# Optimization experiments

Measured on AMD Instinct MI355X. Metric: run time of the kernel, lower is better.

## Reference

```python
import jax, jax.numpy as jnp
import numpy as np

NB, DIM, DSTATE, DCONV, EXPAND = 4, 256, 16, 4, 2
DIN = EXPAND * DIM                 # 512
DTRANK = (DIM + 15) // 16          # 16, mamba-ssm default dt_rank = ceil(d_model/16)
B, L = 16, 512


def layer_norm(x, w, b, eps=1e-5):
    mu = x.mean(-1, keepdims=True)
    var = x.var(-1, keepdims=True)
    return (x - mu) * jax.lax.rsqrt(var + eps) * w + b


def selective_scan(u, delta, A, Bm, Cm, D):
    # u, delta: (B,L,DIN); Bm,Cm: (B,L,N); A: (DIN,N); D: (DIN,)
    def step(h, xs):
        d_t, B_t, C_t, u_t = xs          # (B,DIN), (B,N), (B,N), (B,DIN)
        dA = jnp.exp(d_t[..., None] * A)                                  # (B,DIN,N)
        h = dA * h + d_t[..., None] * B_t[:, None, :] * u_t[..., None]   # (B,DIN,N)
        y = jnp.einsum('bdn,bn->bd', h, C_t)
        return h, y

    h0 = jnp.zeros((u.shape[0], u.shape[2], A.shape[1]), u.dtype)
    xs = (delta.transpose(1, 0, 2), Bm.transpose(1, 0, 2),
          Cm.transpose(1, 0, 2), u.transpose(1, 0, 2))
    _, ys = jax.lax.scan(step, h0, xs)
    return ys.transpose(1, 0, 2) + u * D


def mamba_block(x, ln_w, ln_b, in_w, in_b, cw, cb, xp_w, dtw, dtb, A_log, D, ow):
    h = layer_norm(x, ln_w, ln_b)
    xz = h @ in_w.T + in_b                       # (B,L,2*DIN)
    xin, z = xz[..., :DIN], xz[..., DIN:]
    # causal depthwise conv over the sequence dim
    xc = jax.lax.conv_general_dilated(
        xin.transpose(0, 2, 1), cw[:, None, :], (1,), [(DCONV - 1, 0)],
        dimension_numbers=('NCH', 'OIH', 'NCH'), feature_group_count=DIN)
    xc = jax.nn.silu(xc + cb[None, :, None]).transpose(0, 2, 1)   # (B,L,DIN)
    dbc = xc @ xp_w.T                                             # (B,L,DTRANK+2*N)
    dt = jax.nn.softplus(dbc[..., :DTRANK] @ dtw.T + dtb)         # (B,L,DIN)
    Bm = dbc[..., DTRANK:DTRANK + DSTATE]
    Cm = dbc[..., DTRANK + DSTATE:]
    y = selective_scan(xc, dt, -jnp.exp(A_log), Bm, Cm, D)
    return x + (y * jax.nn.silu(z)) @ ow.T       # dropout = identity at eval


def setup_inputs() -> dict:
    key = jax.random.key(0)
    ks = jax.random.split(key, 8)
    s = 0.02
    A_log = jnp.tile(jnp.log(jnp.arange(1, DSTATE + 1, dtype=jnp.float32))[None, None, :],
                     (NB, DIN, 1))
    return {
        'x': jax.random.normal(ks[0], (B, L, DIM), jnp.float32),
        'ln_w': jnp.ones((NB, DIM), jnp.float32),
        'ln_b': jnp.zeros((NB, DIM), jnp.float32),
        'in_proj_w': jax.random.normal(ks[1], (NB, 2 * DIN, DIM), jnp.float32) * s,
        'in_proj_b': jnp.zeros((NB, 2 * DIN), jnp.float32),
        'conv_w': jax.random.normal(ks[2], (NB, DIN, DCONV), jnp.float32) * s,
        'conv_b': jnp.zeros((NB, DIN), jnp.float32),
        'x_proj_w': jax.random.normal(ks[3], (NB, DTRANK + 2 * DSTATE, DIN), jnp.float32) * s,
        'dt_proj_w': jax.random.normal(ks[4], (NB, DIN, DTRANK), jnp.float32) * s,
        'dt_proj_b': jax.random.uniform(ks[5], (NB, DIN), jnp.float32, -4.0, -3.0),
        'A_log': A_log,
        'D': jnp.ones((NB, DIN), jnp.float32),
        'out_proj_w': jax.random.normal(ks[6], (NB, DIM, DIN), jnp.float32) * s,
    }


def reference(x, ln_w, ln_b, in_proj_w, in_proj_b, conv_w, conv_b, x_proj_w,
              dt_proj_w, dt_proj_b, A_log, D, out_proj_w):
    for i in range(NB):
        x = mamba_block(x, ln_w[i], ln_b[i], in_proj_w[i], in_proj_b[i],
                        conv_w[i], conv_b[i], x_proj_w[i], dt_proj_w[i],
                        dt_proj_b[i], A_log[i], D[i], out_proj_w[i])
    return x
```

## Files before the change

### kernel.cpp

```cpp
#include <hip/hip_runtime.h>
#include <math.h>

#define NB 4
#define DIMM 256
#define DSTATE 16
#define DCONV 4
#define DIN 512
#define DTRANK 16
#define BB 16
#define LL 512
#define TT (BB * LL)
#define XZ_DIM (2 * DIN)
#define DBC_DIM (DTRANK + 2 * DSTATE)
#define NC 32
#define CHUNK (LL / NC)

__device__ __forceinline__ unsigned short f2bf(float f) {
    union { float f; unsigned int u; } v; v.f = f;
    unsigned int r = v.u + 0x7fff + ((v.u >> 16) & 1);
    return (unsigned short)(r >> 16);
}
__device__ __forceinline__ float bf2f(unsigned short u) {
    union { unsigned int i; float f; } v; v.i = ((unsigned int)u) << 16;
    return v.f;
}

__global__ __launch_bounds__(256) void cvt3_kernel(const float* __restrict__ s1,
                                                   unsigned short* __restrict__ d1, int n1,
                                                   const float* __restrict__ s2,
                                                   unsigned short* __restrict__ d2, int n2,
                                                   const float* __restrict__ s3,
                                                   unsigned short* __restrict__ d3, int n3) {
    int stride = gridDim.x * 256;
    for (int i = blockIdx.x * 256 + threadIdx.x; i < n1; i += stride) {
        float4 v = ((const float4*)s1)[i];
        ushort4 o; o.x = f2bf(v.x); o.y = f2bf(v.y); o.z = f2bf(v.z); o.w = f2bf(v.w);
        ((ushort4*)d1)[i] = o;
    }
    for (int i = blockIdx.x * 256 + threadIdx.x; i < n2; i += stride) {
        float4 v = ((const float4*)s2)[i];
        ushort4 o; o.x = f2bf(v.x); o.y = f2bf(v.y); o.z = f2bf(v.z); o.w = f2bf(v.w);
        ((ushort4*)d2)[i] = o;
    }
    for (int i = blockIdx.x * 256 + threadIdx.x; i < n3; i += stride) {
        float4 v = ((const float4*)s3)[i];
        ushort4 o; o.x = f2bf(v.x); o.y = f2bf(v.y); o.z = f2bf(v.z); o.w = f2bf(v.w);
        ((ushort4*)d3)[i] = o;
    }
}

__global__ __launch_bounds__(256) void ln_kernel(const float* __restrict__ x,
                                                 const float* __restrict__ w,
                                                 const float* __restrict__ bvec,
                                                 unsigned short* __restrict__ out) {
    int t = blockIdx.x;
    int i = threadIdx.x;
    float v = x[t * DIMM + i];
    float s = v, s2 = v * v;
#pragma unroll
    for (int off = 1; off < 64; off <<= 1) {
        s  += __shfl_xor(s, off);
        s2 += __shfl_xor(s2, off);
    }
    __shared__ float ss[4], ss2[4];
    int wid = i >> 6;
    if ((i & 63) == 0) { ss[wid] = s; ss2[wid] = s2; }
    __syncthreads();
    s  = ss[0] + ss[1] + ss[2] + ss[3];
    s2 = ss2[0] + ss2[1] + ss2[2] + ss2[3];
    float mu  = s * (1.0f / DIMM);
    float var = s2 * (1.0f / DIMM) - mu * mu;
    float r   = rsqrtf(var + 1e-5f);
    out[t * DIMM + i] = f2bf((v - mu) * r * w[i] + bvec[i]);
}

#define GBM2 128
#define GBN2 128
#define GBK2 32
#define LDW2 (GBK2 + 8)
__global__ __launch_bounds__(256) void gemm128(const unsigned short* __restrict__ A, int lda,
                                               const unsigned short* __restrict__ Bw, int ldb,
                                               const float* __restrict__ bias,
                                               unsigned short* __restrict__ C1b,
                                               unsigned short* __restrict__ C2b, int nsplit,
                                               int ldc, int K) {
    using short8  = __attribute__((ext_vector_type(8))) short;
    using floatx4 = __attribute__((ext_vector_type(4))) float;
    __shared__ __align__(16) unsigned short As[GBM2 * LDW2];
    __shared__ __align__(16) unsigned short Bs[GBN2 * LDW2];

    int tid  = threadIdx.x;
    int m0   = blockIdx.y * GBM2;
    int n0   = blockIdx.x * GBN2;
    int w    = tid >> 6;
    int lane = tid & 63;
    int wm   = (w & 1) * 64;
    int wn   = (w >> 1) * 64;
    int lr   = lane & 15;
    int quad = lane >> 4;

    floatx4 acc[4][4] = {};

    int ar = tid >> 1;
    int ak = (tid & 1) * 16;

    for (int k0 = 0; k0 < K; k0 += GBK2) {
        {
            const unsigned short* src = &A[(size_t)(m0 + ar) * lda + k0 + ak];
            int4 a0 = *(const int4*)(src);
            int4 a1 = *(const int4*)(src + 8);
            *(int4*)&As[ar * LDW2 + ak]     = a0;
            *(int4*)&As[ar * LDW2 + ak + 8] = a1;
        }
        {
            const unsigned short* src = &Bw[(size_t)(n0 + ar) * ldb + k0 + ak];
            int4 b0 = *(const int4*)(src);
            int4 b1 = *(const int4*)(src + 8);
            *(int4*)&Bs[ar * LDW2 + ak]     = b0;
            *(int4*)&Bs[ar * LDW2 + ak + 8] = b1;
        }
        __syncthreads();
        short8 af[4], bf[4];
#pragma unroll
        for (int i = 0; i < 4; ++i)
            af[i] = *(const short8*)&As[(wm + i * 16 + lr) * LDW2 + quad * 8];
#pragma unroll
        for (int j = 0; j < 4; ++j)
            bf[j] = *(const short8*)&Bs[(wn + j * 16 + lr) * LDW2 + quad * 8];
#pragma unroll
        for (int i = 0; i < 4; ++i)
#pragma unroll
            for (int j = 0; j < 4; ++j)
                acc[i][j] = __builtin_amdgcn_mfma_f32_16x16x32_bf16(af[i], bf[j], acc[i][j], 0, 0, 0);
        __syncthreads();
    }

#pragma unroll
    for (int j = 0; j < 4; ++j) {
        int cn = n0 + wn + j * 16 + lr;
        float bb = bias ? bias[cn] : 0.0f;
        unsigned short* dst = (cn < nsplit) ? C1b : C2b;
        int col = (cn < nsplit) ? cn : cn - nsplit;
#pragma unroll
        for (int i = 0; i < 4; ++i)
#pragma unroll
            for (int r = 0; r < 4; ++r) {
                int cm = m0 + wm + i * 16 + quad * 4 + r;
                dst[(size_t)cm * ldc + col] = f2bf(acc[i][j][r] + bb);
            }
    }
}

#define TBM 128
#define TBN 64
#define TBK 32
#define LDKW (TBK + 8)
__global__ __launch_bounds__(256) void gemm_bf16(const unsigned short* __restrict__ A, int lda,
                                                 const unsigned short* __restrict__ Bw, int ldb,
                                                 const float* __restrict__ bias,
                                                 const float* __restrict__ resid,
                                                 float* __restrict__ C,
                                                 unsigned short* __restrict__ C1b,
                                                 unsigned short* __restrict__ C2b, int nsplit,
                                                 int ldc, int N, int K) {
    using short8  = __attribute__((ext_vector_type(8))) short;
    using floatx4 = __attribute__((ext_vector_type(4))) float;
    __shared__ __align__(16) unsigned short As[TBM * LDKW];
    __shared__ __align__(16) unsigned short Bs[TBN * LDKW];

    int tid  = threadIdx.x;
    int m0   = blockIdx.y * TBM;
    int n0   = blockIdx.x * TBN;
    int w    = tid >> 6;
    int lane = tid & 63;
    int wm   = (w & 1) * 64;
    int wn   = (w >> 1) * 32;
    int lr   = lane & 15;
    int quad = lane >> 4;

    floatx4 acc[4][2] = {};

    int ar = tid >> 1;
    int ak = (tid & 1) * 16;
    int br = tid >> 2;
    int bk = (tid & 3) * 8;

    for (int k0 = 0; k0 < K; k0 += TBK) {
        {
            const unsigned short* src = &A[(size_t)(m0 + ar) * lda + k0 + ak];
            int4 a0 = *(const int4*)(src);
            int4 a1 = *(const int4*)(src + 8);
            *(int4*)&As[ar * LDKW + ak]     = a0;
            *(int4*)&As[ar * LDKW + ak + 8] = a1;
        }
        {
            int gn = n0 + br;
            int4 b0 = make_int4(0, 0, 0, 0);
            if (gn < N) b0 = *(const int4*)&Bw[(size_t)gn * ldb + k0 + bk];
            *(int4*)&Bs[br * LDKW + bk] = b0;
        }
        __syncthreads();
        short8 af[4], bf[2];
#pragma unroll
        for (int i = 0; i < 4; ++i)
            af[i] = *(const short8*)&As[(wm + i * 16 + lr) * LDKW + quad * 8];
#pragma unroll
        for (int j = 0; j < 2; ++j)
            bf[j] = *(const short8*)&Bs[(wn + j * 16 + lr) * LDKW + quad * 8];
#pragma unroll
        for (int i = 0; i < 4; ++i)
#pragma unroll
            for (int j = 0; j < 2; ++j)
                acc[i][j] = __builtin_amdgcn_mfma_f32_16x16x32_bf16(af[i], bf[j], acc[i][j], 0, 0, 0);
        __syncthreads();
    }

#pragma unroll
    for (int j = 0; j < 2; ++j) {
        int cn = n0 + wn + j * 16 + lr;
        if (cn < N) {
            float bb = bias ? bias[cn] : 0.0f;
            if (C1b) {
                unsigned short* dst = (cn < nsplit) ? C1b : C2b;
                int col = (cn < nsplit) ? cn : cn - nsplit;
#pragma unroll
                for (int i = 0; i < 4; ++i)
#pragma unroll
                    for (int r = 0; r < 4; ++r) {
                        int cm = m0 + wm + i * 16 + quad * 4 + r;
                        dst[(size_t)cm * ldc + col] = f2bf(acc[i][j][r] + bb);
                    }
            } else {
#pragma unroll
                for (int i = 0; i < 4; ++i)
#pragma unroll
                    for (int r = 0; r < 4; ++r) {
                        int cm = m0 + wm + i * 16 + quad * 4 + r;
                        float v = acc[i][j][r] + bb;
                        if (resid) v += resid[(size_t)cm * ldc + cn];
                        C[(size_t)cm * ldc + cn] = v;
                    }
            }
        }
    }
}

__global__ __launch_bounds__(256) void conv_silu(const unsigned short* __restrict__ Xb,
                                                 const float* __restrict__ cw,
                                                 const float* __restrict__ cb,
                                                 unsigned short* __restrict__ xcb) {
    int idx = blockIdx.x * blockDim.x + threadIdx.x;
    int d = idx & (DIN - 1);
    int t = idx >> 9;
    int l = t & (LL - 1);
    int bq = t >> 9;
    float acc = cb[d];
#pragma unroll
    for (int k = 0; k < DCONV; ++k) {
        int ls = l - (DCONV - 1) + k;
        if (ls >= 0) acc += cw[d * DCONV + k] * bf2f(Xb[(size_t)(bq * LL + ls) * DIN + d]);
    }
    float v = acc / (1.0f + __expf(-acc));
    xcb[(size_t)t * DIN + d] = f2bf(v);
}

__global__ __launch_bounds__(256) void dt_kernel(const float* __restrict__ dbc,
                                                 const float* __restrict__ dtw,
                                                 const float* __restrict__ dtbias,
                                                 unsigned short* __restrict__ dtout) {
    int idx = blockIdx.x * blockDim.x + threadIdx.x;
    int d = idx & (DIN - 1);
    int t = idx >> 9;
    float a = dtbias[d];
    const float4* wv = (const float4*)(dtw + d * DTRANK);
    const float* dr = dbc + (size_t)t * DBC_DIM;
#pragma unroll
    for (int q = 0; q < 4; ++q) {
        float4 w4 = wv[q];
        a += w4.x * dr[q * 4 + 0] + w4.y * dr[q * 4 + 1] +
             w4.z * dr[q * 4 + 2] + w4.w * dr[q * 4 + 3];
    }
    float sp = (a > 20.0f) ? a : log1pf(__expf(a));
    dtout[(size_t)t * DIN + d] = f2bf(sp);
}

__global__ __launch_bounds__(256) void scan_p1(const unsigned short* __restrict__ xcb,
                                               const unsigned short* __restrict__ dtb,
                                               const float* __restrict__ dbc,
                                               const float* __restrict__ A_log,
                                               float* __restrict__ S,
                                               float* __restrict__ H) {
    int bid = blockIdx.x;
    int dq = bid & 3;
    int c  = (bid >> 2) & (NC - 1);
    int b  = bid >> 7;
    int dloc = threadIdx.x >> 1;
    int sh   = threadIdx.x & 1;
    int d  = dq * 128 + dloc;
    int n0 = sh * 8;
    int base = b * LL + c * CHUNK;

    __shared__ float LB[CHUNK * DBC_DIM];
    for (int i = threadIdx.x; i < CHUNK * DBC_DIM / 4; i += 256)
        ((float4*)LB)[i] = ((const float4*)(dbc + (size_t)base * DBC_DIM))[i];

    float a[8];
    {
        const float4* ar = (const float4*)(A_log + d * DSTATE + n0);
        float4 v0 = ar[0], v1 = ar[1];
        a[0] = -__expf(v0.x); a[1] = -__expf(v0.y); a[2] = -__expf(v0.z); a[3] = -__expf(v0.w);
        a[4] = -__expf(v1.x); a[5] = -__expf(v1.y); a[6] = -__expf(v1.z); a[7] = -__expf(v1.w);
    }
    __syncthreads();

    float h[8];
#pragma unroll
    for (int j = 0; j < 8; ++j) h[j] = 0.0f;
    float Ssum = 0.0f;
    float u   = bf2f(xcb[(size_t)base * DIN + d]);
    float dtv = bf2f(dtb[(size_t)base * DIN + d]);
#pragma unroll 4
    for (int s = 0; s < CHUNK; ++s) {
        float nu  = bf2f(xcb[(size_t)(base + s + 1) * DIN + d]);
        float ndt = bf2f(dtb[(size_t)(base + s + 1) * DIN + d]);
        const float* row = &LB[s * DBC_DIM];
        float4 b0 = *(const float4*)&row[DTRANK + n0];
        float4 b1 = *(const float4*)&row[DTRANK + n0 + 4];
        const float btv[8] = {b0.x, b0.y, b0.z, b0.w, b1.x, b1.y, b1.z, b1.w};
        Ssum += dtv;
        float wv = dtv * u;
#pragma unroll
        for (int j = 0; j < 8; ++j) {
            float dA = __expf(dtv * a[j]);
            h[j] = dA * h[j] + wv * btv[j];
        }
        u = nu; dtv = ndt;
    }
    size_t sc = (size_t)b * NC + c;
    if (sh == 0) S[sc * DIN + d] = Ssum;
#pragma unroll
    for (int j = 0; j < 8; ++j) H[(sc * DIN + d) * 16 + n0 + j] = h[j];
}

__global__ __launch_bounds__(256) void scan_p2(const float* __restrict__ A_log,
                                               const float* __restrict__ S,
                                               float* __restrict__ H) {
    int idx = blockIdx.x * 256 + threadIdx.x;
    int n = idx & 15;
    int d = (idx >> 4) & (DIN - 1);
    int b = idx >> 13;
    float a = -__expf(A_log[d * DSTATE + n]);
    float h = 0.0f;
#pragma unroll
    for (int c = 0; c < NC; ++c) {
        size_t sc = (size_t)b * NC + c;
        float Sv = S[sc * DIN + d];
        size_t q = (sc * DIN + d) * 16 + n;
        float Hc = H[q];
        H[q] = h;
        h = __expf(a * Sv) * h + Hc;
    }
}

__global__ __launch_bounds__(256) void scan_p3(const unsigned short* __restrict__ xcb,
                                               const unsigned short* __restrict__ dtb,
                                               const unsigned short* __restrict__ Zb,
                                               const float* __restrict__ dbc,
                                               const float* __restrict__ A_log,
                                               const float* __restrict__ Dp,
                                               const float* __restrict__ Hin,
                                               unsigned short* __restrict__ gb) {
    int bid = blockIdx.x;
    int dq = bid & 3;
    int c  = (bid >> 2) & (NC - 1);
    int b  = bid >> 7;
    int dloc = threadIdx.x >> 1;
    int sh   = threadIdx.x & 1;
    int d  = dq * 128 + dloc;
    int n0 = sh * 8;
    int base = b * LL + c * CHUNK;

    __shared__ float LB[CHUNK * DBC_DIM];
    for (int i = threadIdx.x; i < CHUNK * DBC_DIM / 4; i += 256)
        ((float4*)LB)[i] = ((const float4*)(dbc + (size_t)base * DBC_DIM))[i];

    float a[8];
    {
        const float4* ar = (const float4*)(A_log + d * DSTATE + n0);
        float4 v0 = ar[0], v1 = ar[1];
        a[0] = -__expf(v0.x); a[1] = -__expf(v0.y); a[2] = -__expf(v0.z); a[3] = -__expf(v0.w);
        a[4] = -__expf(v1.x); a[5] = -__expf(v1.y); a[6] = -__expf(v1.z); a[7] = -__expf(v1.w);
    }
    float Dd = Dp[d];
    size_t sc = (size_t)b * NC + c;
    float h[8];
#pragma unroll
    for (int j = 0; j < 8; ++j) h[j] = Hin[(sc * DIN + d) * 16 + n0 + j];
    __syncthreads();

    float u   = bf2f(xcb[(size_t)base * DIN + d]);
    float dtv = bf2f(dtb[(size_t)base * DIN + d]);
#pragma unroll 4
    for (int s = 0; s < CHUNK; ++s) {
        float nu  = bf2f(xcb[(size_t)(base + s + 1) * DIN + d]);
        float ndt = bf2f(dtb[(size_t)(base + s + 1) * DIN + d]);
        const float* row = &LB[s * DBC_DIM];
        float4 b0 = *(const float4*)&row[DTRANK + n0];
        float4 b1 = *(const float4*)&row[DTRANK + n0 + 4];
        float4 c0 = *(const float4*)&row[DTRANK + DSTATE + n0];
        float4 c1 = *(const float4*)&row[DTRANK + DSTATE + n0 + 4];
        const float btv[8] = {b0.x, b0.y, b0.z, b0.w, b1.x, b1.y, b1.z, b1.w};
        const float ctv[8] = {c0.x, c0.y, c0.z, c0.w, c1.x, c1.y, c1.z, c1.w};
        float wv = dtv * u;
        float y  = (sh == 0) ? u * Dd : 0.0f;
#pragma unroll
        for (int j = 0; j < 8; ++j) {
            float dA = __expf(dtv * a[j]);
            h[j] = dA * h[j] + wv * btv[j];
            y += h[j] * ctv[j];
        }
        y += __shfl_xor(y, 1);
        if (sh == 0) {
            float zf = bf2f(Zb[(size_t)(base + s) * DIN + d]);
            float g = y * (zf / (1.0f + __expf(-zf)));
            gb[(size_t)(base + s) * DIN + d] = f2bf(g);
        }
        u = nu; dtv = ndt;
    }
}

extern "C" void kernel_launch(void* const* d_in, const int* in_sizes, int n_in,
                              void* d_out, int out_size, void* d_ws, size_t ws_size,
                              hipStream_t stream) {
    const float* x_in   = (const float*)d_in[0];
    const float* ln_w   = (const float*)d_in[1];
    const float* ln_b   = (const float*)d_in[2];
    const float* in_w   = (const float*)d_in[3];
    const float* in_b   = (const float*)d_in[4];
    const float* conv_w = (const float*)d_in[5];
    const float* conv_b = (const float*)d_in[6];
    const float* xp_w   = (const float*)d_in[7];
    const float* dt_w   = (const float*)d_in[8];
    const float* dt_b   = (const float*)d_in[9];
    const float* A_log  = (const float*)d_in[10];
    const float* Dp     = (const float*)d_in[11];
    const float* ow     = (const float*)d_in[12];
    float* out = (float*)d_out;

    const size_t M = 1048576;
    float* ws = (float*)d_ws;
    float* xbuf = ws;
    unsigned short* hb  = (unsigned short*)(ws + 2 * M);
    float* dbc = ws + 3 * M;
    unsigned short* Xb  = (unsigned short*)(ws + 4 * M);
    unsigned short* Zb  = (unsigned short*)(ws + 6 * M);
    unsigned short* xcb = (unsigned short*)(ws + 8 * M);
    unsigned short* dtb = (unsigned short*)(ws + 10 * M);
    unsigned short* gb  = (unsigned short*)(ws + 12 * M);
    float* Hbuf = ws + 14 * M;
    float* Sbuf = ws + 18 * M;
    unsigned short* inwb = (unsigned short*)(ws + 18 * M + 262144);
    unsigned short* owb  = inwb + (size_t)NB * XZ_DIM * DIMM;
    unsigned short* xpwb = owb + (size_t)NB * DIMM * DIN;

    cvt3_kernel<<<256, 256, 0, stream>>>(
        in_w, inwb, NB * XZ_DIM * DIMM / 4,
        ow,   owb,  NB * DIMM * DIN / 4,
        xp_w, xpwb, NB * DBC_DIM * DIN / 4);

    for (int layer = 0; layer < NB; ++layer) {
        const float* xi = (layer == 0) ? x_in : xbuf;
        float* xo = (layer == NB - 1) ? out : xbuf;

        ln_kernel<<<TT, 256, 0, stream>>>(xi, ln_w + layer * DIMM, ln_b + layer * DIMM, hb);

        gemm128<<<dim3(XZ_DIM / GBN2, TT / GBM2), 256, 0, stream>>>(
            hb, DIMM, inwb + (size_t)layer * XZ_DIM * DIMM, DIMM,
            in_b + layer * XZ_DIM, Xb, Zb, DIN, DIN, DIMM);

        conv_silu<<<(TT * DIN) / 256, 256, 0, stream>>>(
            Xb, conv_w + layer * DIN * DCONV, conv_b + layer * DIN, xcb);

        gemm_bf16<<<dim3(1, TT / TBM), 256, 0, stream>>>(
            xcb, DIN, xpwb + (size_t)layer * DBC_DIM * DIN, DIN,
            nullptr, nullptr, dbc, nullptr, nullptr, 0, DBC_DIM, DBC_DIM, DIN);

        dt_kernel<<<(TT * DIN) / 256, 256, 0, stream>>>(
            dbc, dt_w + (size_t)layer * DIN * DTRANK, dt_b + layer * DIN, dtb);

        const float* Al = A_log + (size_t)layer * DIN * DSTATE;
        scan_p1<<<BB * NC * 4, 256, 0, stream>>>(xcb, dtb, dbc, Al, Sbuf, Hbuf);
        scan_p2<<<(BB * DIN * 16) / 256, 256, 0, stream>>>(Al, Sbuf, Hbuf);
        scan_p3<<<BB * NC * 4, 256, 0, stream>>>(xcb, dtb, Zb, dbc, Al,
                                                 Dp + layer * DIN, Hbuf, gb);

        gemm_bf16<<<dim3(DIMM / TBN, TT / TBM), 256, 0, stream>>>(
            gb, DIN, owb + (size_t)layer * DIMM * DIN, DIN,
            nullptr, xi, xo, nullptr, nullptr, 0, DIMM, DIMM, DIN);
    }
}
```

Before: 679.3 us.

## Fuse dt projection into scan kernels, specialize x/out-proj GEMMs, vectorize layernorm

Measured after the change: 623.0 us. 8.3% less time.

```diff
diff --git a/kernel.cpp b/kernel.cpp
--- a/kernel.cpp
+++ b/kernel.cpp
@@ -49,29 +49,32 @@
     }
 }
 
-__global__ __launch_bounds__(256) void ln_kernel(const float* __restrict__ x,
-                                                 const float* __restrict__ w,
-                                                 const float* __restrict__ bvec,
-                                                 unsigned short* __restrict__ out) {
-    int t = blockIdx.x;
-    int i = threadIdx.x;
-    float v = x[t * DIMM + i];
-    float s = v, s2 = v * v;
+__global__ __launch_bounds__(256) void ln_kernel2(const float* __restrict__ x,
+                                                  const float* __restrict__ w,
+                                                  const float* __restrict__ bvec,
+                                                  unsigned short* __restrict__ out) {
+    int wid  = threadIdx.x >> 6;
+    int lane = threadIdx.x & 63;
+    int t = blockIdx.x * 4 + wid;
+    float4 v = *(const float4*)&x[(size_t)t * DIMM + lane * 4];
+    float s  = v.x + v.y + v.z + v.w;
+    float s2 = v.x * v.x + v.y * v.y + v.z * v.z + v.w * v.w;
 #pragma unroll
     for (int off = 1; off < 64; off <<= 1) {
         s  += __shfl_xor(s, off);
         s2 += __shfl_xor(s2, off);
     }
-    __shared__ float ss[4], ss2[4];
-    int wid = i >> 6;
-    if ((i & 63) == 0) { ss[wid] = s; ss2[wid] = s2; }
-    __syncthreads();
-    s  = ss[0] + ss[1] + ss[2] + ss[3];
-    s2 = ss2[0] + ss2[1] + ss2[2] + ss2[3];
     float mu  = s * (1.0f / DIMM);
     float var = s2 * (1.0f / DIMM) - mu * mu;
     float r   = rsqrtf(var + 1e-5f);
-    out[t * DIMM + i] = f2bf((v - mu) * r * w[i] + bvec[i]);
+    float4 w4 = *(const float4*)&w[lane * 4];
+    float4 b4 = *(const float4*)&bvec[lane * 4];
+    ushort4 o;
+    o.x = f2bf((v.x - mu) * r * w4.x + b4.x);
+    o.y = f2bf((v.y - mu) * r * w4.y + b4.y);
+    o.z = f2bf((v.z - mu) * r * w4.z + b4.z);
+    o.w = f2bf((v.w - mu) * r * w4.w + b4.w);
+    *(ushort4*)&out[(size_t)t * DIMM + lane * 4] = o;
 }
 
 #define GBM2 128
@@ -151,100 +154,6 @@
     }
 }
 
-#define TBM 128
-#define TBN 64
-#define TBK 32
-#define LDKW (TBK + 8)
-__global__ __launch_bounds__(256) void gemm_bf16(const unsigned short* __restrict__ A, int lda,
-                                                 const unsigned short* __restrict__ Bw, int ldb,
-                                                 const float* __restrict__ bias,
-                                                 const float* __restrict__ resid,
-                                                 float* __restrict__ C,
-                                                 unsigned short* __restrict__ C1b,
-                                                 unsigned short* __restrict__ C2b, int nsplit,
-                                                 int ldc, int N, int K) {
-    using short8  = __attribute__((ext_vector_type(8))) short;
-    using floatx4 = __attribute__((ext_vector_type(4))) float;
-    __shared__ __align__(16) unsigned short As[TBM * LDKW];
-    __shared__ __align__(16) unsigned short Bs[TBN * LDKW];
-
-    int tid  = threadIdx.x;
-    int m0   = blockIdx.y * TBM;
-    int n0   = blockIdx.x * TBN;
-    int w    = tid >> 6;
-    int lane = tid & 63;
-    int wm   = (w & 1) * 64;
-    int wn   = (w >> 1) * 32;
-    int lr   = lane & 15;
-    int quad = lane >> 4;
-
-    floatx4 acc[4][2] = {};
-
-    int ar = tid >> 1;
-    int ak = (tid & 1) * 16;
-    int br = tid >> 2;
-    int bk = (tid & 3) * 8;
-
-    for (int k0 = 0; k0 < K; k0 += TBK) {
-        {
-            const unsigned short* src = &A[(size_t)(m0 + ar) * lda + k0 + ak];
-            int4 a0 = *(const int4*)(src);
-            int4 a1 = *(const int4*)(src + 8);
-            *(int4*)&As[ar * LDKW + ak]     = a0;
-            *(int4*)&As[ar * LDKW + ak + 8] = a1;
-        }
-        {
-            int gn = n0 + br;
-            int4 b0 = make_int4(0, 0, 0, 0);
-            if (gn < N) b0 = *(const int4*)&Bw[(size_t)gn * ldb + k0 + bk];
-            *(int4*)&Bs[br * LDKW + bk] = b0;
-        }
-        __syncthreads();
-        short8 af[4], bf[2];
-#pragma unroll
-        for (int i = 0; i < 4; ++i)
-            af[i] = *(const short8*)&As[(wm + i * 16 + lr) * LDKW + quad * 8];
-#pragma unroll
-        for (int j = 0; j < 2; ++j)
-            bf[j] = *(const short8*)&Bs[(wn + j * 16 + lr) * LDKW + quad * 8];
-#pragma unroll
-        for (int i = 0; i < 4; ++i)
-#pragma unroll
-            for (int j = 0; j < 2; ++j)
-                acc[i][j] = __builtin_amdgcn_mfma_f32_16x16x32_bf16(af[i], bf[j], acc[i][j], 0, 0, 0);
-        __syncthreads();
-    }
-
-#pragma unroll
-    for (int j = 0; j < 2; ++j) {
-        int cn = n0 + wn + j * 16 + lr;
-        if (cn < N) {
-            float bb = bias ? bias[cn] : 0.0f;
-            if (C1b) {
-                unsigned short* dst = (cn < nsplit) ? C1b : C2b;
-                int col = (cn < nsplit) ? cn : cn - nsplit;
-#pragma unroll
-                for (int i = 0; i < 4; ++i)
-#pragma unroll
-                    for (int r = 0; r < 4; ++r) {
-                        int cm = m0 + wm + i * 16 + quad * 4 + r;
-                        dst[(size_t)cm * ldc + col] = f2bf(acc[i][j][r] + bb);
-                    }
-            } else {
-#pragma unroll
-                for (int i = 0; i < 4; ++i)
-#pragma unroll
-                    for (int r = 0; r < 4; ++r) {
-                        int cm = m0 + wm + i * 16 + quad * 4 + r;
-                        float v = acc[i][j][r] + bb;
-                        if (resid) v += resid[(size_t)cm * ldc + cn];
-                        C[(size_t)cm * ldc + cn] = v;
-                    }
-            }
-        }
-    }
-}
-
 __global__ __launch_bounds__(256) void conv_silu(const unsigned short* __restrict__ Xb,
                                                  const float* __restrict__ cw,
                                                  const float* __restrict__ cb,
@@ -264,30 +173,115 @@
     xcb[(size_t)t * DIN + d] = f2bf(v);
 }
 
-__global__ __launch_bounds__(256) void dt_kernel(const float* __restrict__ dbc,
-                                                 const float* __restrict__ dtw,
-                                                 const float* __restrict__ dtbias,
-                                                 unsigned short* __restrict__ dtout) {
-    int idx = blockIdx.x * blockDim.x + threadIdx.x;
-    int d = idx & (DIN - 1);
-    int t = idx >> 9;
-    float a = dtbias[d];
-    const float4* wv = (const float4*)(dtw + d * DTRANK);
-    const float* dr = dbc + (size_t)t * DBC_DIM;
-#pragma unroll
-    for (int q = 0; q < 4; ++q) {
-        float4 w4 = wv[q];
-        a += w4.x * dr[q * 4 + 0] + w4.y * dr[q * 4 + 1] +
-             w4.z * dr[q * 4 + 2] + w4.w * dr[q * 4 + 3];
-    }
-    float sp = (a > 20.0f) ? a : log1pf(__expf(a));
-    dtout[(size_t)t * DIN + d] = f2bf(sp);
+#define XPM 64
+__global__ __launch_bounds__(256) void xproj_gemm(const unsigned short* __restrict__ A,
+                                                  const unsigned short* __restrict__ Bw,
+                                                  float* __restrict__ dbc) {
+    using short8  = __attribute__((ext_vector_type(8))) short;
+    using floatx4 = __attribute__((ext_vector_type(4))) float;
+    __shared__ __align__(16) unsigned short As[XPM * DIN];
+    __shared__ __align__(16) unsigned short Bs[48 * DIN];
+
+    int tid = threadIdx.x;
+    int m0  = blockIdx.x * XPM;
+#pragma unroll
+    for (int t = 0; t < 16; ++t) {
+        int i = tid + t * 256;
+        int r = i >> 6, c = i & 63;
+        int col = (c * 8) ^ ((r & 7) << 3);
+        *(int4*)&As[r * DIN + col] = *(const int4*)&A[(size_t)(m0 + r) * DIN + c * 8];
+    }
+#pragma unroll
+    for (int t = 0; t < 12; ++t) {
+        int i = tid + t * 256;
+        int r = i >> 6, c = i & 63;
+        int col = (c * 8) ^ ((r & 7) << 3);
+        *(int4*)&Bs[r * DIN + col] = *(const int4*)&Bw[(size_t)r * DIN + c * 8];
+    }
+    __syncthreads();
+
+    int w = tid >> 6, lane = tid & 63, lr = lane & 15, quad = lane >> 4;
+    int wm = w * 16;
+    floatx4 acc[3] = {};
+#pragma unroll
+    for (int k0 = 0; k0 < DIN; k0 += 32) {
+        int ca = (k0 + quad * 8) ^ ((lr & 7) << 3);
+        short8 af = *(const short8*)&As[(wm + lr) * DIN + ca];
+        short8 b0 = *(const short8*)&Bs[(0  + lr) * DIN + ca];
+        short8 b1 = *(const short8*)&Bs[(16 + lr) * DIN + ca];
+        short8 b2 = *(const short8*)&Bs[(32 + lr) * DIN + ca];
+        acc[0] = __builtin_amdgcn_mfma_f32_16x16x32_bf16(af, b0, acc[0], 0, 0, 0);
+        acc[1] = __builtin_amdgcn_mfma_f32_16x16x32_bf16(af, b1, acc[1], 0, 0, 0);
+        acc[2] = __builtin_amdgcn_mfma_f32_16x16x32_bf16(af, b2, acc[2], 0, 0, 0);
+    }
+#pragma unroll
+    for (int j = 0; j < 3; ++j) {
+        int cn = j * 16 + lr;
+#pragma unroll
+        for (int r = 0; r < 4; ++r) {
+            int row = wm + quad * 4 + r;
+            dbc[(size_t)(m0 + row) * DBC_DIM + cn] = acc[j][r];
+        }
+    }
+}
+
+__global__ __launch_bounds__(256) void oproj_gemm(const unsigned short* __restrict__ A,
+                                                  const unsigned short* __restrict__ Bw,
+                                                  const float* __restrict__ resid,
+                                                  float* __restrict__ C) {
+    using short8  = __attribute__((ext_vector_type(8))) short;
+    using floatx4 = __attribute__((ext_vector_type(4))) float;
+    __shared__ __align__(16) unsigned short As[64 * DIN];
+    __shared__ __align__(16) unsigned short Bs[64 * DIN];
+
+    int tid = threadIdx.x;
+    int m0  = blockIdx.y * 64;
+    int n0  = blockIdx.x * 64;
+#pragma unroll
+    for (int t = 0; t < 16; ++t) {
+        int i = tid + t * 256;
+        int r = i >> 6, c = i & 63;
+        int col = (c * 8) ^ ((r & 7) << 3);
+        *(int4*)&As[r * DIN + col] = *(const int4*)&A[(size_t)(m0 + r) * DIN + c * 8];
+    }
+#pragma unroll
+    for (int t = 0; t < 16; ++t) {
+        int i = tid + t * 256;
+        int r = i >> 6, c = i & 63;
+        int col = (c * 8) ^ ((r & 7) << 3);
+        *(int4*)&Bs[r * DIN + col] = *(const int4*)&Bw[(size_t)(n0 + r) * DIN + c * 8];
+    }
+    __syncthreads();
+
+    int w = tid >> 6, lane = tid & 63, lr = lane & 15, quad = lane >> 4;
+    int wm = w * 16;
+    floatx4 acc[4] = {};
+#pragma unroll
+    for (int k0 = 0; k0 < DIN; k0 += 32) {
+        int ca = (k0 + quad * 8) ^ ((lr & 7) << 3);
+        short8 af = *(const short8*)&As[(wm + lr) * DIN + ca];
+#pragma unroll
+        for (int j = 0; j < 4; ++j) {
+            short8 bf = *(const short8*)&Bs[(j * 16 + lr) * DIN + ca];
+            acc[j] = __builtin_amdgcn_mfma_f32_16x16x32_bf16(af, bf, acc[j], 0, 0, 0);
+        }
+    }
+#pragma unroll
+    for (int j = 0; j < 4; ++j) {
+        int cn = n0 + j * 16 + lr;
+#pragma unroll
+        for (int r = 0; r < 4; ++r) {
+            int cm = m0 + wm + quad * 4 + r;
+            C[(size_t)cm * DIMM + cn] = acc[j][r] + resid[(size_t)cm * DIMM + cn];
+        }
+    }
 }
 
 __global__ __launch_bounds__(256) void scan_p1(const unsigned short* __restrict__ xcb,
-                                               const unsigned short* __restrict__ dtb,
                                                const float* __restrict__ dbc,
                                                const float* __restrict__ A_log,
+                                               const float* __restrict__ dtw,
+                                               const float* __restrict__ dtbias,
                                                float* __restrict__ S,
                                                float* __restrict__ H) {
     int bid = blockIdx.x;
@@ -301,6 +295,7 @@
     int base = b * LL + c * CHUNK;
 
     __shared__ float LB[CHUNK * DBC_DIM];
+    __shared__ float DT[CHUNK * 128];
     for (int i = threadIdx.x; i < CHUNK * DBC_DIM / 4; i += 256)
         ((float4*)LB)[i] = ((const float4*)(dbc + (size_t)base * DBC_DIM))[i];
 
@@ -313,16 +308,36 @@
     }
     __syncthreads();
 
+    {
+        int dl = threadIdx.x & 127;
+        int dd = dq * 128 + dl;
+        const float4* wv = (const float4*)(dtw + (size_t)dd * DTRANK);
+        float4 w0 = wv[0], w1 = wv[1], w2 = wv[2], w3 = wv[3];
+        float bias = dtbias[dd];
+#pragma unroll
+        for (int k = 0; k < 8; ++k) {
+            int t = (threadIdx.x >> 7) + k * 2;
+            const float* dr = &LB[t * DBC_DIM];
+            float av = bias;
+            av += w0.x * dr[0]  + w0.y * dr[1]  + w0.z * dr[2]  + w0.w * dr[3];
+            av += w1.x * dr[4]  + w1.y * dr[5]  + w1.z * dr[6]  + w1.w * dr[7];
+            av += w2.x * dr[8]  + w2.y * dr[9]  + w2.z * dr[10] + w2.w * dr[11];
+            av += w3.x * dr[12] + w3.y * dr[13] + w3.z * dr[14] + w3.w * dr[15];
+            float sp = (av > 20.0f) ? av : log1pf(__expf(av));
+            DT[t * 128 + dl] = bf2f(f2bf(sp));
+        }
+    }
+    __syncthreads();
+
     float h[8];
 #pragma unroll
     for (int j = 0; j < 8; ++j) h[j] = 0.0f;
     float Ssum = 0.0f;
-    float u   = bf2f(xcb[(size_t)base * DIN + d]);
-    float dtv = bf2f(dtb[(size_t)base * DIN + d]);
+    float u = bf2f(xcb[(size_t)base * DIN + d]);
 #pragma unroll 4
     for (int s = 0; s < CHUNK; ++s) {
         float nu  = bf2f(xcb[(size_t)(base + s + 1) * DIN + d]);
-        float ndt = bf2f(dtb[(size_t)(base + s + 1) * DIN + d]);
+        float dtv = DT[s * 128 + dloc];
         const float* row = &LB[s * DBC_DIM];
         float4 b0 = *(const float4*)&row[DTRANK + n0];
         float4 b1 = *(const float4*)&row[DTRANK + n0 + 4];
@@ -334,7 +349,7 @@
             float dA = __expf(dtv * a[j]);
             h[j] = dA * h[j] + wv * btv[j];
         }
-        u = nu; dtv = ndt;
+        u = nu;
     }
     size_t sc = (size_t)b * NC + c;
     if (sh == 0) S[sc * DIN + d] = Ssum;
@@ -363,10 +378,11 @@
 }
 
 __global__ __launch_bounds__(256) void scan_p3(const unsigned short* __restrict__ xcb,
-                                               const unsigned short* __restrict__ dtb,
                                                const unsigned short* __restrict__ Zb,
                                                const float* __restrict__ dbc,
                                                const float* __restrict__ A_log,
+                                               const float* __restrict__ dtw,
+                                               const float* __restrict__ dtbias,
                                                const float* __restrict__ Dp,
                                                const float* __restrict__ Hin,
                                                unsigned short* __restrict__ gb) {
@@ -381,6 +397,7 @@
     int base = b * LL + c * CHUNK;
 
     __shared__ float LB[CHUNK * DBC_DIM];
+    __shared__ float DT[CHUNK * 128];
     for (int i = threadIdx.x; i < CHUNK * DBC_DIM / 4; i += 256)
         ((float4*)LB)[i] = ((const float4*)(dbc + (size_t)base * DBC_DIM))[i];
 
@@ -398,12 +415,32 @@
     for (int j = 0; j < 8; ++j) h[j] = Hin[(sc * DIN + d) * 16 + n0 + j];
     __syncthreads();
 
-    float u   = bf2f(xcb[(size_t)base * DIN + d]);
-    float dtv = bf2f(dtb[(size_t)base * DIN + d]);
+    {
+        int dl = threadIdx.x & 127;
+        int dd = dq * 128 + dl;
+        const float4* wv = (const float4*)(dtw + (size_t)dd * DTRANK);
+        float4 w0 = wv[0], w1 = wv[1], w2 = wv[2], w3 = wv[3];
+        float bias = dtbias[dd];
+#pragma unroll
+        for (int k = 0; k < 8; ++k) {
+            int t = (threadIdx.x >> 7) + k * 2;
+            const float* dr = &LB[t * DBC_DIM];
+            float av = bias;
+            av += w0.x * dr[0]  + w0.y * dr[1]  + w0.z * dr[2]  + w0.w * dr[3];
+            av += w1.x * dr[4]  + w1.y * dr[5]  + w1.z * dr[6]  + w1.w * dr[7];
+            av += w2.x * dr[8]  + w2.y * dr[9]  + w2.z * dr[10] + w2.w * dr[11];
+            av += w3.x * dr[12] + w3.y * dr[13] + w3.z * dr[14] + w3.w * dr[15];
+            float sp = (av > 20.0f) ? av : log1pf(__expf(av));
+            DT[t * 128 + dl] = bf2f(f2bf(sp));
+        }
+    }
+    __syncthreads();
+
+    float u = bf2f(xcb[(size_t)base * DIN + d]);
 #pragma unroll 4
     for (int s = 0; s < CHUNK; ++s) {
         float nu  = bf2f(xcb[(size_t)(base + s + 1) * DIN + d]);
-        float ndt = bf2f(dtb[(size_t)(base + s + 1) * DIN + d]);
+        float dtv = DT[s * 128 + dloc];
         const float* row = &LB[s * DBC_DIM];
         float4 b0 = *(const float4*)&row[DTRANK + n0];
         float4 b1 = *(const float4*)&row[DTRANK + n0 + 4];
@@ -425,7 +462,7 @@
             float g = y * (zf / (1.0f + __expf(-zf)));
             gb[(size_t)(base + s) * DIN + d] = f2bf(g);
         }
-        u = nu; dtv = ndt;
+        u = nu;
     }
 }
 
@@ -455,7 +492,6 @@
     unsigned short* Xb  = (unsigned short*)(ws + 4 * M);
     unsigned short* Zb  = (unsigned short*)(ws + 6 * M);
     unsigned short* xcb = (unsigned short*)(ws + 8 * M);
-    unsigned short* dtb = (unsigned short*)(ws + 10 * M);
     unsigned short* gb  = (unsigned short*)(ws + 12 * M);
     float* Hbuf = ws + 14 * M;
     float* Sbuf = ws + 18 * M;
@@ -472,7 +508,7 @@
         const float* xi = (layer == 0) ? x_in : xbuf;
         float* xo = (layer == NB - 1) ? out : xbuf;
 
-        ln_kernel<<<TT, 256, 0, stream>>>(xi, ln_w + layer * DIMM, ln_b + layer * DIMM, hb);
+        ln_kernel2<<<TT / 4, 256, 0, stream>>>(xi, ln_w + layer * DIMM, ln_b + layer * DIMM, hb);
 
         gemm128<<<dim3(XZ_DIM / GBN2, TT / GBM2), 256, 0, stream>>>(
             hb, DIMM, inwb + (size_t)layer * XZ_DIM * DIMM, DIMM,
@@ -481,21 +517,18 @@
         conv_silu<<<(TT * DIN) / 256, 256, 0, stream>>>(
             Xb, conv_w + layer * DIN * DCONV, conv_b + layer * DIN, xcb);
 
-        gemm_bf16<<<dim3(1, TT / TBM), 256, 0, stream>>>(
-            xcb, DIN, xpwb + (size_t)layer * DBC_DIM * DIN, DIN,
-            nullptr, nullptr, dbc, nullptr, nullptr, 0, DBC_DIM, DBC_DIM, DIN);
-
-        dt_kernel<<<(TT * DIN) / 256, 256, 0, stream>>>(
-            dbc, dt_w + (size_t)layer * DIN * DTRANK, dt_b + layer * DIN, dtb);
+        xproj_gemm<<<TT / XPM, 256, 0, stream>>>(
+            xcb, xpwb + (size_t)layer * DBC_DIM * DIN, dbc);
 
         const float* Al = A_log + (size_t)layer * DIN * DSTATE;
-        scan_p1<<<BB * NC * 4, 256, 0, stream>>>(xcb, dtb, dbc, Al, Sbuf, Hbuf);
+        const float* dtwL = dt_w + (size_t)layer * DIN * DTRANK;
+        const float* dtbL = dt_b + layer * DIN;
+        scan_p1<<<BB * NC * 4, 256, 0, stream>>>(xcb, dbc, Al, dtwL, dtbL, Sbuf, Hbuf);
         scan_p2<<<(BB * DIN * 16) / 256, 256, 0, stream>>>(Al, Sbuf, Hbuf);
-        scan_p3<<<BB * NC * 4, 256, 0, stream>>>(xcb, dtb, Zb, dbc, Al,
+        scan_p3<<<BB * NC * 4, 256, 0, stream>>>(xcb, Zb, dbc, Al, dtwL, dtbL,
                                                  Dp + layer * DIN, Hbuf, gb);
 
-        gemm_bf16<<<dim3(DIMM / TBN, TT / TBM), 256, 0, stream>>>(
-            gb, DIN, owb + (size_t)layer * DIMM * DIN, DIN,
-            nullptr, xi, xo, nullptr, nullptr, 0, DIMM, DIMM, DIN);
-    }
-}
+        oproj_gemm<<<dim3(DIMM / 64, TT / 64), 256, 0, stream>>>(
+            gb, owb + (size_t)layer * DIMM * DIN, xi, xo);
+    }
+}
```
